# Optimization experiments

Hardware: AMD Instinct MI355X
Metric: run time of the kernel (lower is better)

## Reference

```python
import jax, jax.numpy as jnp
import numpy as np

C = 32          # in_channels = out_channels = groups
K = 3           # kernel_size
STRIDE = 2
PAD = 1
DIL = 1
EPS = 1e-20


def _depthwise_convT(x, w):
    """Equivalent of torch.F.conv_transpose2d(x, w, groups=C, stride=STRIDE,
    padding=PAD, dilation=DIL) with w of shape (C, 1, K, K).
    Implemented as an lhs-dilated conv with a spatially flipped kernel."""
    w_f = w[:, :, ::-1, ::-1]
    pad = DIL * (K - 1) - PAD  # = 1 for K=3, PAD=1, DIL=1
    return jax.lax.conv_general_dilated(
        x, w_f,
        window_strides=(1, 1),
        padding=[(pad, pad), (pad, pad)],
        lhs_dilation=(STRIDE, STRIDE),
        rhs_dilation=(DIL, DIL),
        dimension_numbers=('NCHW', 'OIHW', 'NCHW'),
        feature_group_count=C)


def setup_inputs() -> dict:
    key = jax.random.key(0)
    k = jax.random.split(key, 7)
    B, H, W = 2, 176, 608
    # depths/confidences are positive (rand); gy is signed (randn)
    d = jax.random.uniform(k[0], (B, C, H, W), dtype=jnp.float32) + 0.5
    cd = jax.random.uniform(k[1], (B, C, H, W), dtype=jnp.float32)
    gy = jax.random.normal(k[2], (B, C, H, W), dtype=jnp.float32)
    cgy = jax.random.uniform(k[3], (B, C, H, W), dtype=jnp.float32)
    w_prop_raw = jax.random.normal(k[4], (1, C, 1, 1), dtype=jnp.float32)
    spatial_weight_raw = jax.random.normal(k[5], (C, 1, K, K), dtype=jnp.float32)
    bias = 0.01 * jax.random.normal(k[6], (1, C, 1, 1), dtype=jnp.float32)
    return {"d": d, "cd": cd, "gy": gy, "cgy": cgy,
            "w_prop_raw": w_prop_raw,
            "spatial_weight_raw": spatial_weight_raw,
            "bias": bias}


def reference(d, cd, gy, cgy, w_prop_raw, spatial_weight_raw, bias):
    # EnforcePos('softplus') on both learned weights
    w_prop = jax.nn.softplus(w_prop_raw)          # (1, C, 1, 1)
    sw = jax.nn.softplus(spatial_weight_raw)      # (C, 1, K, K)

    # roll-based vertical neighbor gather with edge confidence zeroing
    d_up = jnp.roll(d, 1, axis=2)
    cd_up = jnp.roll(cd, 1, axis=2).at[:, :, 0, :].set(0.0)
    d_down = jnp.roll(d, -1, axis=2)
    cd_down = jnp.roll(cd, -1, axis=2).at[:, :, -1, :].set(0.0)

    cgy_from_ds = cd_up * cd_up
    height = (cd_up * d_up + cd_down * d_down) / (cd_up + cd_down)
    gy_from_ds = (d_down - d_up) / 2.0 / height

    gy_f = (w_prop * cgy * gy + cgy_from_ds * gy_from_ds) / (w_prop * cgy + cgy_from_ds)
    cgy_f = (w_prop * cgy + cgy_from_ds) / (w_prop + 1.0)

    nom = _depthwise_convT(cgy_f * gy_f, sw)
    denom = _depthwise_convT(cgy_f, sw)
    cdenom = _depthwise_convT(jnp.ones_like(cgy_f), sw)

    # original adds bias twice: once unconditionally, once under use_bias
    gy_out = nom / (denom + EPS) + bias + bias
    cgy_out = denom / (cdenom + EPS)
    return gy_out / STRIDE, cgy_out
```

## Files before the change

kernel.cpp:

```cpp
#include <hip/hip_runtime.h>
#include <math.h>

#define B_   2
#define C_   32
#define H_   176
#define W_   608
#define HO_  351
#define WO_  1215
#define PLANE_O (HO_ * WO_)
#define OUT1_O  (B_ * C_ * PLANE_O)
#define EPS_ 1e-20f
#define NTH  512
#define W4   (W_ / 4)
#define HW_  304
#define NRLDS 9

typedef float f4_t __attribute__((ext_vector_type(4)));
typedef float f2_t __attribute__((ext_vector_type(2)));

__device__ __forceinline__ float softplus_f(float x) {
    return fmaxf(x, 0.0f) + log1pf(expf(-fabsf(x)));
}

extern "C" __global__ __launch_bounds__(NTH, 6)
void structn_pipe(const float* __restrict__ d,
                  const float* __restrict__ cd,
                  const float* __restrict__ gy,
                  const float* __restrict__ cgy,
                  const float* __restrict__ wpr,
                  const float* __restrict__ swr,
                  const float* __restrict__ bias,
                  float* __restrict__ out)
{
    __shared__ float s_nE[NRLDS * HW_];
    __shared__ float s_nO[NRLDS * HW_];
    __shared__ float s_cE[NRLDS * HW_];
    __shared__ float s_cO[NRLDS * HW_];

    const int G     = blockIdx.x;
    const int plane = blockIdx.y;
    const int c     = plane & (C_ - 1);

    float sw[9];
#pragma unroll
    for (int k = 0; k < 9; ++k) sw[k] = softplus_f(swr[c * 9 + k]);
    const float wp      = softplus_f(wpr[c]);
    const float inv_wp1 = 1.0f / (wp + 1.0f);
    const float bv      = bias[c];
    const float icd_ee  = 1.0f / (sw[4] + EPS_);
    const float icd_eo  = 1.0f / (sw[3] + sw[5] + EPS_);
    const float icd_oe  = 1.0f / (sw[1] + sw[7] + EPS_);
    const float icd_oo  = 1.0f / (sw[0] + sw[2] + sw[6] + sw[8] + EPS_);

    const int f0 = G * 8;

    const int pbase = plane * (H_ * W_);
    const float* __restrict__ dP  = d   + pbase;
    const float* __restrict__ cdP = cd  + pbase;
    const float* __restrict__ gyP = gy  + pbase;
    const float* __restrict__ cgP = cgy + pbase;

    auto stage_rows = [&](int j0, int j1) {
        const int ntask = (j1 - j0) * W4;
        for (int idx = threadIdx.x; idx < ntask; idx += NTH) {
            const int rf = j0 + idx / W4;
            const int iw = (idx - (rf - j0) * W4) << 2;
            const int iy = f0 + rf;
            const int up = (iy == 0)      ? (H_ - 1) : iy - 1;
            const int dn = (iy == H_ - 1) ? 0        : iy + 1;
            const float mu = (iy > 0)      ? 1.0f : 0.0f;
            const float md = (iy < H_ - 1) ? 1.0f : 0.0f;

            const f4_t du = *(const f4_t*)(dP  + up * W_ + iw);
            const f4_t dd = *(const f4_t*)(dP  + dn * W_ + iw);
            const f4_t cu = *(const f4_t*)(cdP + up * W_ + iw);
            const f4_t cn = *(const f4_t*)(cdP + dn * W_ + iw);
            const f4_t gg = *(const f4_t*)(gyP + iy * W_ + iw);
            const f4_t cg = *(const f4_t*)(cgP + iy * W_ + iw);

            f4_t sn4, sc4;
#pragma unroll
            for (int e = 0; e < 4; ++e) {
                const float cuv = cu[e] * mu;
                const float cnv = cn[e] * md;
                const float cfd = cuv * cuv;
                const float rs  = __builtin_amdgcn_rcpf(fmaf(cuv, du[e], cnv * dd[e]));
                const float gfd = 0.5f * (dd[e] - du[e]) * (cuv + cnv) * rs;
                const float num = fmaf(wp * cg[e], gg[e], cfd * gfd);
                const float den = fmaf(wp, cg[e], cfd);
                sn4[e] = num * inv_wp1;
                sc4[e] = den * inv_wp1;
            }
            const int eo = rf * HW_ + (iw >> 1);
            f2_t v;
            v[0] = sn4[0]; v[1] = sn4[2];  *(f2_t*)(s_nE + eo) = v;
            v[0] = sn4[1]; v[1] = sn4[3];  *(f2_t*)(s_nO + eo) = v;
            v[0] = sc4[0]; v[1] = sc4[2];  *(f2_t*)(s_cE + eo) = v;
            v[0] = sc4[1]; v[1] = sc4[3];  *(f2_t*)(s_cO + eo) = v;
        }
    };

    const int w    = threadIdx.x >> 6;
    const int lane = threadIdx.x & 63;

    auto consume_half = [&](int h) {
        const int oy = G * 16 + 8 * h + w;
        if (oy >= HO_) return;

        const int p   = w & 1;
        const int lrA = 4 * h + (w >> 1);

        const int ro0 = plane * PLANE_O + oy * WO_;
        float* __restrict__ o0 = out + ro0;
        float* __restrict__ o1 = out + OUT1_O + ro0;

        const int h4 = (4 - (ro0 & 3)) & 3;
        const int n4 = (WO_ - h4) >> 2;
        const int q  = h4 & 1;
        const int r  = (h4 >> 1) & 1;

        const float icdC = p ? icd_oe : icd_ee;
        const float icdO = p ? icd_oo : icd_eo;
        const float i0 = q ? icdO : icdC;
        const float i1 = q ? icdC : icdO;

        const float* __restrict__ nAE = s_nE + lrA * HW_;
        const float* __restrict__ nAO = s_nO + lrA * HW_;
        const float* __restrict__ cAE = s_cE + lrA * HW_;
        const float* __restrict__ cAO = s_cO + lrA * HW_;

#define VAL(E, O, j) (((j) & 1) ? (O)[((j) - 1) >> 1] : (E)[(j) >> 1])
        if (p == 0) {
            if (lane < 3) {
                const int ox = (lane < h4) ? lane : (h4 + (n4 << 2) + lane - h4);
                float den, nom, icd;
                if ((ox & 1) == 0) {
                    const int j = ox >> 1;
                    den = VAL(cAE, cAO, j) * sw[4];
                    nom = VAL(nAE, nAO, j) * sw[4];
                    icd = icd_ee;
                } else {
                    const int j = (ox - 1) >> 1;
                    den = VAL(cAE, cAO, j) * sw[5] + VAL(cAE, cAO, j + 1) * sw[3];
                    nom = VAL(nAE, nAO, j) * sw[5] + VAL(nAE, nAO, j + 1) * sw[3];
                    icd = icd_eo;
                }
                o0[ox] = fmaf(0.5f * nom, __builtin_amdgcn_rcpf(den + EPS_), bv);
                o1[ox] = den * icd;
            }
            const float* pa0 = r ? nAO : nAE;
            const float* pa1 = r ? nAE + 1 : nAO;
            const float* pa2 = r ? nAO + 1 : nAE + 1;
            const float* px0 = r ? cAO : cAE;
            const float* px1 = r ? cAE + 1 : cAO;
            const float* px2 = r ? cAO + 1 : cAE + 1;

            for (int k = lane; k < n4; k += 64) {
                const float a0 = pa0[k], a1 = pa1[k], a2 = pa2[k];
                const float x0 = px0[k], x1 = px1[k], x2 = px2[k];
                const float dC0 = x0 * sw[4], dC1 = x1 * sw[4], dC2 = x2 * sw[4];
                const float nC0 = a0 * sw[4], nC1 = a1 * sw[4], nC2 = a2 * sw[4];
                const float dF0 = x0 * sw[5] + x1 * sw[3];
                const float dF1 = x1 * sw[5] + x2 * sw[3];
                const float nF0 = a0 * sw[5] + a1 * sw[3];
                const float nF1 = a1 * sw[5] + a2 * sw[3];

                const float d0 = q ? dF0 : dC0, n0 = q ? nF0 : nC0;
                const float d1 = q ? dC1 : dF0, n1 = q ? nC1 : nF0;
                const float d2 = q ? dF1 : dC1, n2 = q ? nF1 : nC1;
                const float d3 = q ? dC2 : dF1, n3 = q ? nC2 : nF1;

                f4_t gv, qv;
                gv[0] = fmaf(0.5f * n0, __builtin_amdgcn_rcpf(d0 + EPS_), bv);
                gv[1] = fmaf(0.5f * n1, __builtin_amdgcn_rcpf(d1 + EPS_), bv);
                gv[2] = fmaf(0.5f * n2, __builtin_amdgcn_rcpf(d2 + EPS_), bv);
                gv[3] = fmaf(0.5f * n3, __builtin_amdgcn_rcpf(d3 + EPS_), bv);
                qv[0] = d0 * i0; qv[1] = d1 * i1; qv[2] = d2 * i0; qv[3] = d3 * i1;

                const int c0 = h4 + (k << 2);
                __builtin_nontemporal_store(gv, (f4_t*)(o0 + c0));
                __builtin_nontemporal_store(qv, (f4_t*)(o1 + c0));
            }
        } else {
            const float* __restrict__ nBE = nAE + HW_;
            const float* __restrict__ nBO = nAO + HW_;
            const float* __restrict__ cBE = cAE + HW_;
            const float* __restrict__ cBO = cAO + HW_;

            if (lane < 3) {
                const int ox = (lane < h4) ? lane : (h4 + (n4 << 2) + lane - h4);
                float den, nom, icd;
                if ((ox & 1) == 0) {
                    const int j = ox >> 1;
                    den = VAL(cAE, cAO, j) * sw[7] + VAL(cBE, cBO, j) * sw[1];
                    nom = VAL(nAE, nAO, j) * sw[7] + VAL(nBE, nBO, j) * sw[1];
                    icd = icd_oe;
                } else {
                    const int j = (ox - 1) >> 1;
                    den = VAL(cAE, cAO, j) * sw[8] + VAL(cAE, cAO, j + 1) * sw[6]
                        + VAL(cBE, cBO, j) * sw[2] + VAL(cBE, cBO, j + 1) * sw[0];
                    nom = VAL(nAE, nAO, j) * sw[8] + VAL(nAE, nAO, j + 1) * sw[6]
                        + VAL(nBE, nBO, j) * sw[2] + VAL(nBE, nBO, j + 1) * sw[0];
                    icd = icd_oo;
                }
                o0[ox] = fmaf(0.5f * nom, __builtin_amdgcn_rcpf(den + EPS_), bv);
                o1[ox] = den * icd;
            }

            const float* pa0 = r ? nAO : nAE;
            const float* pa1 = r ? nAE + 1 : nAO;
            const float* pa2 = r ? nAO + 1 : nAE + 1;
            const float* px0 = r ? cAO : cAE;
            const float* px1 = r ? cAE + 1 : cAO;
            const float* px2 = r ? cAO + 1 : cAE + 1;
            const float* pb0 = r ? nBO : nBE;
            const float* pb1 = r ? nBE + 1 : nBO;
            const float* pb2 = r ? nBO + 1 : nBE + 1;
            const float* py0 = r ? cBO : cBE;
            const float* py1 = r ? cBE + 1 : cBO;
            const float* py2 = r ? cBO + 1 : cBE + 1;

            for (int k = lane; k < n4; k += 64) {
                const float a0 = pa0[k], a1 = pa1[k], a2 = pa2[k];
                const float x0 = px0[k], x1 = px1[k], x2 = px2[k];
                const float b0 = pb0[k], b1 = pb1[k], b2 = pb2[k];
                const float y0 = py0[k], y1 = py1[k], y2 = py2[k];

                const float dC0 = x0 * sw[7] + y0 * sw[1];
                const float dC1 = x1 * sw[7] + y1 * sw[1];
                const float dC2 = x2 * sw[7] + y2 * sw[1];
                const float nC0 = a0 * sw[7] + b0 * sw[1];
                const float nC1 = a1 * sw[7] + b1 * sw[1];
                const float nC2 = a2 * sw[7] + b2 * sw[1];
                const float dF0 = x0 * sw[8] + x1 * sw[6] + y0 * sw[2] + y1 * sw[0];
                const float dF1 = x1 * sw[8] + x2 * sw[6] + y1 * sw[2] + y2 * sw[0];
                const float nF0 = a0 * sw[8] + a1 * sw[6] + b0 * sw[2] + b1 * sw[0];
                const float nF1 = a1 * sw[8] + a2 * sw[6] + b1 * sw[2] + b2 * sw[0];

                const float d0 = q ? dF0 : dC0, n0 = q ? nF0 : nC0;
                const float d1 = q ? dC1 : dF0, n1 = q ? nC1 : nF0;
                const float d2 = q ? dF1 : dC1, n2 = q ? nF1 : nC1;
                const float d3 = q ? dC2 : dF1, n3 = q ? nC2 : nF1;

                f4_t gv, qv;
                gv[0] = fmaf(0.5f * n0, __builtin_amdgcn_rcpf(d0 + EPS_), bv);
                gv[1] = fmaf(0.5f * n1, __builtin_amdgcn_rcpf(d1 + EPS_), bv);
                gv[2] = fmaf(0.5f * n2, __builtin_amdgcn_rcpf(d2 + EPS_), bv);
                gv[3] = fmaf(0.5f * n3, __builtin_amdgcn_rcpf(d3 + EPS_), bv);
                qv[0] = d0 * i0; qv[1] = d1 * i1; qv[2] = d2 * i0; qv[3] = d3 * i1;

                const int c0 = h4 + (k << 2);
                __builtin_nontemporal_store(gv, (f4_t*)(o0 + c0));
                __builtin_nontemporal_store(qv, (f4_t*)(o1 + c0));
            }
        }
#undef VAL
    };

    stage_rows(0, 5);
    __syncthreads();
    stage_rows(5, min(NRLDS, H_ - f0));
    consume_half(0);
    __syncthreads();
    consume_half(1);
}

extern "C" void kernel_launch(void* const* d_in, const int* in_sizes, int n_in,
                              void* d_out, int out_size, void* d_ws, size_t ws_size,
                              hipStream_t stream) {
    const float* d    = (const float*)d_in[0];
    const float* cd   = (const float*)d_in[1];
    const float* gy   = (const float*)d_in[2];
    const float* cgy  = (const float*)d_in[3];
    const float* wpr  = (const float*)d_in[4];
    const float* swr  = (const float*)d_in[5];
    const float* bias = (const float*)d_in[6];
    float* out = (float*)d_out;

    dim3 grid(22, B_ * C_);
    structn_pipe<<<grid, NTH, 0, stream>>>(d, cd, gy, cgy, wpr, swr, bias, out);
}
```

Baseline: 68.70 us.

## Halve row tile per block and split each output row across two waves

Each block now stages 5 input rows instead of 9 and produces 8 output rows instead of 16. The grid doubles to 44 blocks per plane. Each output row is shared by two waves that stride the columns by 128. Smaller LDS use and a higher launch-bounds occupancy target aim to fit more blocks per CU and give better latency hiding and tail balance. The cost is a larger halo overhead: overlapping rows are re-read relatively more often, and the softplus setup is repeated in twice as many blocks.

```diff
diff --git a/kernel.cpp b/kernel.cpp
--- a/kernel.cpp
+++ b/kernel.cpp
@@ -13,7 +13,7 @@
 #define NTH  512
 #define W4   (W_ / 4)
 #define HW_  304
-#define NRLDS 9
+#define NRLDS 5
 
 typedef float f4_t __attribute__((ext_vector_type(4)));
 typedef float f2_t __attribute__((ext_vector_type(2)));
@@ -22,15 +22,15 @@
     return fmaxf(x, 0.0f) + log1pf(expf(-fabsf(x)));
 }
 
-extern "C" __global__ __launch_bounds__(NTH, 6)
-void structn_pipe(const float* __restrict__ d,
-                  const float* __restrict__ cd,
-                  const float* __restrict__ gy,
-                  const float* __restrict__ cgy,
-                  const float* __restrict__ wpr,
-                  const float* __restrict__ swr,
-                  const float* __restrict__ bias,
-                  float* __restrict__ out)
+extern "C" __global__ __launch_bounds__(NTH, 8)
+void structn_pipe8(const float* __restrict__ d,
+                   const float* __restrict__ cd,
+                   const float* __restrict__ gy,
+                   const float* __restrict__ cgy,
+                   const float* __restrict__ wpr,
+                   const float* __restrict__ swr,
+                   const float* __restrict__ bias,
+                   float* __restrict__ out)
 {
     __shared__ float s_nE[NRLDS * HW_];
     __shared__ float s_nO[NRLDS * HW_];
@@ -52,7 +52,7 @@
     const float icd_oe  = 1.0f / (sw[1] + sw[7] + EPS_);
     const float icd_oo  = 1.0f / (sw[0] + sw[2] + sw[6] + sw[8] + EPS_);
 
-    const int f0 = G * 8;
+    const int f0 = G * 4;
 
     const int pbase = plane * (H_ * W_);
     const float* __restrict__ dP  = d   + pbase;
@@ -61,7 +61,8 @@
     const float* __restrict__ cgP = cgy + pbase;
 
     auto stage_rows = [&](int j0, int j1) {
-        const int ntask = (j1 - j0) * W4;
+        const int j1c = min(j1, H_ - f0);
+        const int ntask = (j1c > j0) ? (j1c - j0) * W4 : 0;
         for (int idx = threadIdx.x; idx < ntask; idx += NTH) {
             const int rf = j0 + idx / W4;
             const int iw = (idx - (rf - j0) * W4) << 2;
@@ -103,12 +104,14 @@
     const int w    = threadIdx.x >> 6;
     const int lane = threadIdx.x & 63;
 
-    auto consume_half = [&](int h) {
-        const int oy = G * 16 + 8 * h + w;
+    auto consume_quarter = [&](int qi) {
+        const int rr = w >> 1;
+        const int s  = w & 1;
+        const int oy = G * 8 + 4 * qi + rr;
         if (oy >= HO_) return;
 
-        const int p   = w & 1;
-        const int lrA = 4 * h + (w >> 1);
+        const int p   = rr & 1;
+        const int lrA = 2 * qi + (rr >> 1);
 
         const int ro0 = plane * PLANE_O + oy * WO_;
         float* __restrict__ o0 = out + ro0;
@@ -131,7 +134,7 @@
 
 #define VAL(E, O, j) (((j) & 1) ? (O)[((j) - 1) >> 1] : (E)[(j) >> 1])
         if (p == 0) {
-            if (lane < 3) {
+            if (s == 0 && lane < 3) {
                 const int ox = (lane < h4) ? lane : (h4 + (n4 << 2) + lane - h4);
                 float den, nom, icd;
                 if ((ox & 1) == 0) {
@@ -155,7 +158,7 @@
             const float* px1 = r ? cAE + 1 : cAO;
             const float* px2 = r ? cAO + 1 : cAE + 1;
 
-            for (int k = lane; k < n4; k += 64) {
+            for (int k = lane + 64 * s; k < n4; k += 128) {
                 const float a0 = pa0[k], a1 = pa1[k], a2 = pa2[k];
                 const float x0 = px0[k], x1 = px1[k], x2 = px2[k];
                 const float dC0 = x0 * sw[4], dC1 = x1 * sw[4], dC2 = x2 * sw[4];
@@ -187,7 +190,7 @@
             const float* __restrict__ cBE = cAE + HW_;
             const float* __restrict__ cBO = cAO + HW_;
 
-            if (lane < 3) {
+            if (s == 0 && lane < 3) {
                 const int ox = (lane < h4) ? lane : (h4 + (n4 << 2) + lane - h4);
                 float den, nom, icd;
                 if ((ox & 1) == 0) {
@@ -220,7 +223,7 @@
             const float* py1 = r ? cBE + 1 : cBO;
             const float* py2 = r ? cBO + 1 : cBE + 1;
 
-            for (int k = lane; k < n4; k += 64) {
+            for (int k = lane + 64 * s; k < n4; k += 128) {
                 const float a0 = pa0[k], a1 = pa1[k], a2 = pa2[k];
                 const float x0 = px0[k], x1 = px1[k], x2 = px2[k];
                 const float b0 = pb0[k], b1 = pb1[k], b2 = pb2[k];
@@ -257,12 +260,12 @@
 #undef VAL
     };
 
-    stage_rows(0, 5);
+    stage_rows(0, 3);
     __syncthreads();
-    stage_rows(5, min(NRLDS, H_ - f0));
-    consume_half(0);
+    stage_rows(3, NRLDS);
+    consume_quarter(0);
     __syncthreads();
-    consume_half(1);
+    consume_quarter(1);
 }
 
 extern "C" void kernel_launch(void* const* d_in, const int* in_sizes, int n_in,
@@ -277,6 +280,6 @@
     const float* bias = (const float*)d_in[6];
     float* out = (float*)d_out;
 
-    dim3 grid(22, B_ * C_);
-    structn_pipe<<<grid, NTH, 0, stream>>>(d, cd, gy, cgy, wpr, swr, bias, out);
+    dim3 grid(44, B_ * C_);
+    structn_pipe8<<<grid, NTH, 0, stream>>>(d, cd, gy, cgy, wpr, swr, bias, out);
 }
```

After: 76.58 us. 1.11x slower.

## Warp-specialize block: producer warps stage rows while consumer warps write outputs

Applied to the files above, without the earlier changes.

Splits the 8 wavefronts into 6 consumer waves that compute output rows and 2 producer waves that stage the next input rows into LDS, in three phases separated by barriers. The final phase uses all waves, two per output row. The goal is to overlap global loads for later rows with output computation and stores, where before all threads staged and then all consumed. The cost is an extra barrier and fewer threads doing the staging loads, which could leave the producer phase as the bottleneck.

```diff
diff --git a/kernel.cpp b/kernel.cpp
--- a/kernel.cpp
+++ b/kernel.cpp
@@ -23,14 +23,14 @@
 }
 
 extern "C" __global__ __launch_bounds__(NTH, 6)
-void structn_pipe(const float* __restrict__ d,
-                  const float* __restrict__ cd,
-                  const float* __restrict__ gy,
-                  const float* __restrict__ cgy,
-                  const float* __restrict__ wpr,
-                  const float* __restrict__ swr,
-                  const float* __restrict__ bias,
-                  float* __restrict__ out)
+void structn_ws(const float* __restrict__ d,
+                const float* __restrict__ cd,
+                const float* __restrict__ gy,
+                const float* __restrict__ cgy,
+                const float* __restrict__ wpr,
+                const float* __restrict__ swr,
+                const float* __restrict__ bias,
+                float* __restrict__ out)
 {
     __shared__ float s_nE[NRLDS * HW_];
     __shared__ float s_nO[NRLDS * HW_];
@@ -60,9 +60,10 @@
     const float* __restrict__ gyP = gy  + pbase;
     const float* __restrict__ cgP = cgy + pbase;
 
-    auto stage_rows = [&](int j0, int j1) {
-        const int ntask = (j1 - j0) * W4;
-        for (int idx = threadIdx.x; idx < ntask; idx += NTH) {
+    auto stage_rows = [&](int j0, int j1, int tid, int tstep) {
+        const int j1c = min(j1, H_ - f0);
+        const int ntask = (j1c > j0) ? (j1c - j0) * W4 : 0;
+        for (int idx = tid; idx < ntask; idx += tstep) {
             const int rf = j0 + idx / W4;
             const int iw = (idx - (rf - j0) * W4) << 2;
             const int iy = f0 + rf;
@@ -103,21 +104,21 @@
     const int w    = threadIdx.x >> 6;
     const int lane = threadIdx.x & 63;
 
-    auto consume_half = [&](int h) {
-        const int oy = G * 16 + 8 * h + w;
+    auto consume_row = [&](int oyl, int kbase, int kstep) {
+        const int oy = G * 16 + oyl;
         if (oy >= HO_) return;
 
-        const int p   = w & 1;
-        const int lrA = 4 * h + (w >> 1);
+        const int p   = oyl & 1;
+        const int lrA = oyl >> 1;
 
         const int ro0 = plane * PLANE_O + oy * WO_;
         float* __restrict__ o0 = out + ro0;
         float* __restrict__ o1 = out + OUT1_O + ro0;
 
-        const int h4 = (4 - (ro0 & 3)) & 3;
-        const int n4 = (WO_ - h4) >> 2;
-        const int q  = h4 & 1;
-        const int r  = (h4 >> 1) & 1;
+        const int hd = (4 - (ro0 & 3)) & 3;
+        const int n4 = (WO_ - hd) >> 2;
+        const int q  = hd & 1;
+        const int r  = (hd >> 1) & 1;
 
         const float icdC = p ? icd_oe : icd_ee;
         const float icdO = p ? icd_oo : icd_eo;
@@ -131,8 +132,8 @@
 
 #define VAL(E, O, j) (((j) & 1) ? (O)[((j) - 1) >> 1] : (E)[(j) >> 1])
         if (p == 0) {
-            if (lane < 3) {
-                const int ox = (lane < h4) ? lane : (h4 + (n4 << 2) + lane - h4);
+            if (kbase == 0 && lane < 3) {
+                const int ox = (lane < hd) ? lane : (hd + (n4 << 2) + lane - hd);
                 float den, nom, icd;
                 if ((ox & 1) == 0) {
                     const int j = ox >> 1;
@@ -155,7 +156,7 @@
             const float* px1 = r ? cAE + 1 : cAO;
             const float* px2 = r ? cAO + 1 : cAE + 1;
 
-            for (int k = lane; k < n4; k += 64) {
+            for (int k = kbase + lane; k < n4; k += kstep) {
                 const float a0 = pa0[k], a1 = pa1[k], a2 = pa2[k];
                 const float x0 = px0[k], x1 = px1[k], x2 = px2[k];
                 const float dC0 = x0 * sw[4], dC1 = x1 * sw[4], dC2 = x2 * sw[4];
@@ -177,7 +178,7 @@
                 gv[3] = fmaf(0.5f * n3, __builtin_amdgcn_rcpf(d3 + EPS_), bv);
                 qv[0] = d0 * i0; qv[1] = d1 * i1; qv[2] = d2 * i0; qv[3] = d3 * i1;
 
-                const int c0 = h4 + (k << 2);
+                const int c0 = hd + (k << 2);
                 __builtin_nontemporal_store(gv, (f4_t*)(o0 + c0));
                 __builtin_nontemporal_store(qv, (f4_t*)(o1 + c0));
             }
@@ -187,8 +188,8 @@
             const float* __restrict__ cBE = cAE + HW_;
             const float* __restrict__ cBO = cAO + HW_;
 
-            if (lane < 3) {
-                const int ox = (lane < h4) ? lane : (h4 + (n4 << 2) + lane - h4);
+            if (kbase == 0 && lane < 3) {
+                const int ox = (lane < hd) ? lane : (hd + (n4 << 2) + lane - hd);
                 float den, nom, icd;
                 if ((ox & 1) == 0) {
                     const int j = ox >> 1;
@@ -220,7 +221,7 @@
             const float* py1 = r ? cBE + 1 : cBO;
             const float* py2 = r ? cBO + 1 : cBE + 1;
 
-            for (int k = lane; k < n4; k += 64) {
+            for (int k = kbase + lane; k < n4; k += kstep) {
                 const float a0 = pa0[k], a1 = pa1[k], a2 = pa2[k];
                 const float x0 = px0[k], x1 = px1[k], x2 = px2[k];
                 const float b0 = pb0[k], b1 = pb1[k], b2 = pb2[k];
@@ -249,7 +250,7 @@
                 gv[3] = fmaf(0.5f * n3, __builtin_amdgcn_rcpf(d3 + EPS_), bv);
                 qv[0] = d0 * i0; qv[1] = d1 * i1; qv[2] = d2 * i0; qv[3] = d3 * i1;
 
-                const int c0 = h4 + (k << 2);
+                const int c0 = hd + (k << 2);
                 __builtin_nontemporal_store(gv, (f4_t*)(o0 + c0));
                 __builtin_nontemporal_store(qv, (f4_t*)(o1 + c0));
             }
@@ -257,12 +258,15 @@
 #undef VAL
     };
 
-    stage_rows(0, 5);
+    stage_rows(0, 4, threadIdx.x, NTH);
     __syncthreads();
-    stage_rows(5, min(NRLDS, H_ - f0));
-    consume_half(0);
+    if (w < 6) consume_row(w, 0, 64);
+    else       stage_rows(4, 7, threadIdx.x - 384, 128);
     __syncthreads();
-    consume_half(1);
+    if (w < 6) consume_row(6 + w, 0, 64);
+    else       stage_rows(7, 9, threadIdx.x - 384, 128);
+    __syncthreads();
+    consume_row(12 + (w >> 1), 64 * (w & 1), 128);
 }
 
 extern "C" void kernel_launch(void* const* d_in, const int* in_sizes, int n_in,
@@ -278,5 +282,5 @@
     float* out = (float*)d_out;
 
     dim3 grid(22, B_ * C_);
-    structn_pipe<<<grid, NTH, 0, stream>>>(d, cd, gy, cgy, wpr, swr, bias, out);
+    structn_ws<<<grid, NTH, 0, stream>>>(d, cd, gy, cgy, wpr, swr, bias, out);
 }
```

After: 70.60 us. 2.8% more time.
